# Optimization experiments

Measured on AMD Instinct MI355X. Metric: run time of the kernel, lower is better.

The kernel has to match this reference:

```python
import jax, jax.numpy as jnp
import numpy as np

N = 50000      # nodes
E = 800000     # edges (before self loops)
IN = 128       # in_channels
HID = 64       # hidden_channels
HEADS = 4      # num_heads
OUT = 40       # out_channels
NEG_SLOPE = 0.2


def setup_inputs() -> dict:
    key = jax.random.key(0)
    ks = jax.random.split(key, 16)
    x = jax.random.normal(ks[0], (N, IN), dtype=jnp.float32)
    edge_index = jax.random.randint(ks[1], (2, E), 0, N, dtype=jnp.int64)

    def lin(k, fan_in, fan_out):
        return jax.random.normal(k, (fan_in, fan_out), dtype=jnp.float32) * (1.0 / np.sqrt(fan_in))

    def att(k, h, c):
        return jax.random.normal(k, (h, c), dtype=jnp.float32) * (1.0 / np.sqrt(c))

    return {
        "x": x, "edge_index": edge_index,
        "W1": lin(ks[2], IN, HEADS * HID),
        "as1": att(ks[3], HEADS, HID), "ad1": att(ks[4], HEADS, HID),
        "b1": jnp.zeros((HEADS * HID,), jnp.float32),
        "W2": lin(ks[5], HEADS * HID, HEADS * HID),
        "as2": att(ks[6], HEADS, HID), "ad2": att(ks[7], HEADS, HID),
        "b2": jnp.zeros((HEADS * HID,), jnp.float32),
        "W3": lin(ks[8], HEADS * HID, OUT),
        "as3": att(ks[9], 1, OUT), "ad3": att(ks[10], 1, OUT),
        "b3": jnp.zeros((OUT,), jnp.float32),
    }


def _gat_layer(x, src, dst, W, a_src, a_dst, b):
    """One GATConv: linear -> per-edge attention -> segment softmax -> scatter-sum."""
    n = x.shape[0]
    H, C = a_src.shape
    h = (x @ W).reshape(n, H, C)                       # [N,H,C]
    al_s = jnp.einsum('nhc,hc->nh', h, a_src)          # [N,H]
    al_d = jnp.einsum('nhc,hc->nh', h, a_dst)          # [N,H]
    alpha = jax.nn.leaky_relu(al_s[src] + al_d[dst], NEG_SLOPE)  # [Etot,H]
    m = jax.ops.segment_max(alpha, dst, num_segments=n)          # stable softmax over incoming edges
    e = jnp.exp(alpha - m[dst])
    denom = jax.ops.segment_sum(e, dst, num_segments=n)
    attn = e / denom[dst]                              # [Etot,H]
    out = jax.ops.segment_sum(h[src] * attn[:, :, None], dst, num_segments=n)  # [N,H,C]
    return out.reshape(n, H * C) + b


def reference(x, edge_index, W1, as1, ad1, b1, W2, as2, ad2, b2, W3, as3, ad3, b3):
    # add self loops once (PyG GATConv default add_self_loops=True)
    loops = jnp.arange(N, dtype=edge_index.dtype)
    src = jnp.concatenate([edge_index[0], loops])
    dst = jnp.concatenate([edge_index[1], loops])

    h = _gat_layer(x, src, dst, W1, as1, ad1, b1)
    h = jax.nn.relu(h)                                 # dropout is identity in eval mode
    h = _gat_layer(h, src, dst, W2, as2, ad2, b2)
    h = jax.nn.relu(h)
    h = _gat_layer(h, src, dst, W3, as3, ad3, b3)      # final layer: 1 head
    return jax.nn.log_softmax(h, axis=-1)
```

## Files before the change

kernel.cpp:

```cpp
#include <hip/hip_runtime.h>
#include <math.h>

#define N_NODES 50000
#define N_EDGES 800000
#define ETOT    (N_EDGES + N_NODES)
#define EPAD_MAX 1200000
#define IN_CH   128
#define OUT_CH  40
#define NEG     0.2f
#define CAP     64

#define NPF   98
#define NFINE 512
#define FCAP  2400

typedef __attribute__((ext_vector_type(8))) short bf16x8;
typedef __attribute__((ext_vector_type(4))) float f32x4;
typedef __attribute__((ext_vector_type(2))) float f32x2;

__device__ inline unsigned short f2bf(float f) {
    unsigned int u = __float_as_uint(f);
    return (unsigned short)((u + 0x7FFFu + ((u >> 16) & 1u)) >> 16);
}
__device__ inline float bf2f(unsigned short u) {
    return __uint_as_float((unsigned int)u << 16);
}
__device__ inline float lrelu(float a) { return (a > 0.f) ? a : NEG * a; }

__global__ __launch_bounds__(256) void k_bkt(const int* __restrict__ ei,
                                             int* __restrict__ fcur,
                                             unsigned int* __restrict__ fbuf,
                                             const float* __restrict__ W1,
                                             const float* __restrict__ W2,
                                             const float* __restrict__ W3,
                                             unsigned short* __restrict__ Wt1,
                                             unsigned short* __restrict__ Wt2,
                                             unsigned short* __restrict__ Wt3) {
    if (blockIdx.x >= 256) {
        int i = (blockIdx.x - 256) * 256 + threadIdx.x;
        if (i < 32768) {
            int n = i >> 7, k = i & 127;
            Wt1[i] = f2bf(W1[(long)k * 256 + n]);
        } else if (i < 98304) {
            int j = i - 32768;
            int n = j >> 8, k = j & 255;
            Wt2[j] = f2bf(W2[(long)k * 256 + n]);
        } else if (i < 114688) {
            int j = i - 98304;
            int n = j >> 8, k = j & 255;
            Wt3[j] = (n < OUT_CH) ? f2bf(W3[(long)k * OUT_CH + n]) : (unsigned short)0;
        }
        return;
    }
    __shared__ int lcnt[NFINE], lbase[NFINE], lcur[NFINE];
    int tid = threadIdx.x;
    for (int i = tid; i < NFINE; i += 256) lcnt[i] = 0;
    __syncthreads();
    for (int i = blockIdx.x * 256 + tid; i < ETOT; i += 256 * 256) {
        int d = (i < N_EDGES) ? ei[N_EDGES + i] : (i - N_EDGES);
        atomicAdd(&lcnt[d / NPF], 1);
    }
    __syncthreads();
    for (int i = tid; i < NFINE; i += 256) {
        lbase[i] = atomicAdd(&fcur[i], lcnt[i]);
        lcur[i] = 0;
    }
    __syncthreads();
    for (int i = blockIdx.x * 256 + tid; i < ETOT; i += 256 * 256) {
        int s, d;
        if (i < N_EDGES) { s = ei[i]; d = ei[N_EDGES + i]; }
        else             { s = i - N_EDGES; d = s; }
        int p = d / NPF;
        int off = atomicAdd(&lcur[p], 1);
        fbuf[(long)p * FCAP + lbase[p] + off] = (unsigned int)s | ((unsigned int)d << 16);
    }
}

__global__ __launch_bounds__(256) void k_build(const int* __restrict__ fcur,
                                               const unsigned int* __restrict__ fbuf,
                                               int* __restrict__ deg,
                                               int* __restrict__ gcur,
                                               int* __restrict__ start,
                                               int* __restrict__ eSrc) {
    __shared__ int cnt[NPF];
    __shared__ int sval[128];
    __shared__ int offs[NPF];
    __shared__ int base_[NPF];
    __shared__ int pbase;
    int f = blockIdx.x;
    int tid = threadIdx.x;
    int n0 = f * NPF;
    int nend = min(n0 + NPF, N_NODES);
    int nn = nend - n0;
    if (tid < NPF) cnt[tid] = 0;
    __syncthreads();
    int n = fcur[f];
    for (int i = tid; i < n; i += 256)
        atomicAdd(&cnt[(int)(fbuf[(long)f * FCAP + i] >> 16) - n0], 1);
    __syncthreads();
    int pd = 0;
    if (tid < 128) {
        pd = (tid < nn) ? ((cnt[tid] + 7) & ~7) : 0;
        sval[tid] = pd;
    }
    __syncthreads();
    #pragma unroll
    for (int off = 1; off < 128; off <<= 1) {
        int t = 0;
        if (tid < 128 && tid >= off) t = sval[tid - off];
        __syncthreads();
        if (tid < 128) sval[tid] += t;
        __syncthreads();
    }
    if (tid == 0) pbase = atomicAdd(gcur, sval[127]);
    __syncthreads();
    if (tid < nn) {
        int st = pbase + sval[tid] - pd;
        deg[n0 + tid] = cnt[tid];
        start[n0 + tid] = st;
        offs[tid] = st;
        base_[tid] = st;
    }
    __syncthreads();
    for (int i = tid; i < n; i += 256) {
        unsigned int u = fbuf[(long)f * FCAP + i];
        int d = (int)(u >> 16);
        int pos = atomicAdd(&offs[d - n0], 1);
        eSrc[pos] = (int)(u & 0xFFFFu);
    }
    __syncthreads();
    if (tid < nn) {
        int endp = offs[tid];
        int dg = endp - base_[tid];
        int stop = base_[tid] + ((dg + 7) & ~7);
        for (int k2 = endp; k2 < stop; ++k2) eSrc[k2] = -1;
    }
}

#define PITCH 40
template<int BN, int FM, int FN, bool CVT, bool FP8OUT, bool L4>
__global__ __launch_bounds__(256) void k_mfma(const void* __restrict__ Araw,
                                              const unsigned short* __restrict__ Bt,
                                              void* __restrict__ Cout,
                                              const float* __restrict__ a_s,
                                              const float* __restrict__ a_d,
                                              float* __restrict__ als,
                                              float* __restrict__ ald,
                                              int M, int K, int Ncol) {
    __shared__ unsigned short As[128 * PITCH];
    __shared__ unsigned short Bs[BN * PITCH];
    const int WCOLS = BN / (FN * 16);
    int tid = threadIdx.x;
    int wave = tid >> 6, lane = tid & 63;
    int quad = lane >> 4, l16 = lane & 15;
    int wr = wave / WCOLS, wc = wave % WCOLS;
    long row0 = (long)blockIdx.x * 128;
    int col0 = blockIdx.y * BN;

    f32x4 acc[FM][FN] = {};

    for (int k0 = 0; k0 < K; k0 += 32) {
        for (int c = tid; c < 512; c += 256) {
            int r = c >> 2, kp = (c & 3) << 3;
            long gr = row0 + r;
            if (CVT) {
                const float* A32 = (const float*)Araw;
                ushort4 lo = {0,0,0,0}, hi = {0,0,0,0};
                if (gr < M) {
                    float4 v0 = *(const float4*)(A32 + gr * K + k0 + kp);
                    float4 v1 = *(const float4*)(A32 + gr * K + k0 + kp + 4);
                    lo.x = f2bf(v0.x); lo.y = f2bf(v0.y); lo.z = f2bf(v0.z); lo.w = f2bf(v0.w);
                    hi.x = f2bf(v1.x); hi.y = f2bf(v1.y); hi.z = f2bf(v1.z); hi.w = f2bf(v1.w);
                }
                *(ushort4*)(As + r * PITCH + kp) = lo;
                *(ushort4*)(As + r * PITCH + kp + 4) = hi;
            } else {
                const unsigned short* A16 = (const unsigned short*)Araw;
                uint4 v = {0u, 0u, 0u, 0u};
                if (gr < M) v = *(const uint4*)(A16 + gr * K + k0 + kp);
                *(uint4*)(As + r * PITCH + kp) = v;
            }
        }
        for (int c = tid; c < BN * 4; c += 256) {
            int r = c >> 2, kp = (c & 3) << 3;
            uint4 v = *(const uint4*)(Bt + (long)(col0 + r) * K + k0 + kp);
            *(uint4*)(Bs + r * PITCH + kp) = v;
        }
        __syncthreads();
        bf16x8 af[FM], bfr[FN];
        #pragma unroll
        for (int i = 0; i < FM; ++i)
            af[i] = *(const bf16x8*)(As + (wr * FM * 16 + i * 16 + l16) * PITCH + quad * 8);
        #pragma unroll
        for (int j = 0; j < FN; ++j)
            bfr[j] = *(const bf16x8*)(Bs + (wc * FN * 16 + j * 16 + l16) * PITCH + quad * 8);
        #pragma unroll
        for (int i = 0; i < FM; ++i)
            #pragma unroll
            for (int j = 0; j < FN; ++j)
                acc[i][j] = __builtin_amdgcn_mfma_f32_16x16x32_bf16(af[i], bfr[j], acc[i][j], 0, 0, 0);
        __syncthreads();
    }

    {
        int head = L4 ? (blockIdx.y * WCOLS + wc) : 0;
        float as_v[FN], ad_v[FN];
        #pragma unroll
        for (int j = 0; j < FN; ++j) {
            int cidx = j * 16 + l16;
            if (L4) {
                as_v[j] = a_s[head * 64 + cidx];
                ad_v[j] = a_d[head * 64 + cidx];
            } else {
                as_v[j] = (cidx < OUT_CH) ? a_s[cidx] : 0.f;
                ad_v[j] = (cidx < OUT_CH) ? a_d[cidx] : 0.f;
            }
        }
        #pragma unroll
        for (int i = 0; i < FM; ++i) {
            #pragma unroll
            for (int v = 0; v < 4; ++v) {
                float ps = acc[i][0][v] * as_v[0] + acc[i][1][v] * as_v[1]
                         + acc[i][2][v] * as_v[2] + acc[i][3][v] * as_v[3];
                float pd = acc[i][0][v] * ad_v[0] + acc[i][1][v] * ad_v[1]
                         + acc[i][2][v] * ad_v[2] + acc[i][3][v] * ad_v[3];
                #pragma unroll
                for (int off = 1; off < 16; off <<= 1) {
                    ps += __shfl_xor(ps, off);
                    pd += __shfl_xor(pd, off);
                }
                if (l16 == 0) {
                    long row = row0 + wr * (FM * 16) + i * 16 + quad * 4 + v;
                    if (row < M) {
                        if (L4) { als[row * 4 + head] = ps; ald[row * 4 + head] = pd; }
                        else    { als[row] = ps; ald[row] = pd; }
                    }
                }
            }
        }
    }

    if (FP8OUT) {
        unsigned char* C8 = (unsigned char*)Cout;
        #pragma unroll
        for (int i = 0; i < FM; ++i) {
            #pragma unroll
            for (int v = 0; v < 4; ++v) {
                long row = row0 + wr * FM * 16 + i * 16 + quad * 4 + v;
                if (row < M) {
                    int p01 = __builtin_amdgcn_cvt_pk_fp8_f32(acc[i][0][v], acc[i][1][v], 0, false);
                    int p23 = __builtin_amdgcn_cvt_pk_fp8_f32(acc[i][2][v], acc[i][3][v], 0, false);
                    unsigned char* b = C8 + row * 256 + col0 + wc * (FN * 16) + l16;
                    b[0]  = (unsigned char)(p01 & 0xFF);
                    b[16] = (unsigned char)((p01 >> 8) & 0xFF);
                    b[32] = (unsigned char)(p23 & 0xFF);
                    b[48] = (unsigned char)((p23 >> 8) & 0xFF);
                }
            }
        }
    } else {
        unsigned short* C = (unsigned short*)Cout;
        #pragma unroll
        for (int i = 0; i < FM; ++i) {
            long rowb = row0 + wr * FM * 16 + i * 16 + quad * 4;
            #pragma unroll
            for (int j = 0; j < FN; ++j) {
                int col = col0 + wc * FN * 16 + j * 16 + l16;
                if (col < Ncol) {
                    #pragma unroll
                    for (int v = 0; v < 4; ++v) {
                        long r = rowb + v;
                        if (r < M) C[r * Ncol + col] = f2bf(acc[i][j][v]);
                    }
                }
            }
        }
    }
}

__global__ __launch_bounds__(256) void k_agg4(const unsigned char* __restrict__ h8,
                                              const int* __restrict__ start,
                                              const int* __restrict__ deg,
                                              const int* __restrict__ eSrc,
                                              const float* __restrict__ als,
                                              const float* __restrict__ ald,
                                              const float* __restrict__ bias,
                                              unsigned short* __restrict__ out) {
    __shared__ float wbuf[4][CAP * 4];
    __shared__ int   sbuf[4][CAP];
    int wid = threadIdx.x >> 6;
    int node = (blockIdx.x * blockDim.x + threadIdx.x) >> 6;
    int lane = threadIdx.x & 63;
    if (node >= N_NODES) return;
    int st = start[node];
    int dgp = (deg[node] + 7) & ~7;
    const int* ep = eSrc + st;

    int l16 = lane & 15, headw = lane >> 4;
    float aldd4 = ald[node * 4 + headw];
    int ncap = (dgp < CAP) ? dgp : CAP;
    for (int c = 0; c < ncap; c += 16) {
        int slot = c + l16;
        bool ok = (slot < ncap);
        int raw = ok ? ep[slot] : -1;
        int ss = (raw < 0) ? 0 : raw;
        float a = als[(long)ss * 4 + headw] + aldd4;
        float w = (raw < 0) ? 0.f : __expf(lrelu(a));
        if (ok) {
            wbuf[wid][slot * 4 + headw] = w;
            if (headw == 0) sbuf[wid][slot] = ss << 8;
        }
    }

    int q = lane >> 4;
    int head = l16 >> 2;
    const unsigned char* hb = h8 + l16 * 16;
    float den = 0.f;
    f32x2 acc2[8] = {};

    for (int j = 0; j < ncap; j += 8) {
        int  s0 = sbuf[wid][j + q];
        int  s1 = sbuf[wid][j + 4 + q];
        float w0 = wbuf[wid][(j + q) * 4 + head];
        float w1 = wbuf[wid][(j + 4 + q) * 4 + head];
        uint4 h0 = *(const uint4*)(hb + (long)s0);
        uint4 h1 = *(const uint4*)(hb + (long)s1);
        den += w0 + w1;
        f32x2 W0; W0.x = w0; W0.y = w0;
        f32x2 W1; W1.x = w1; W1.y = w1;
        acc2[0] += W0 * __builtin_amdgcn_cvt_pk_f32_fp8((int)h0.x, false);
        acc2[1] += W0 * __builtin_amdgcn_cvt_pk_f32_fp8((int)h0.x, true);
        acc2[2] += W0 * __builtin_amdgcn_cvt_pk_f32_fp8((int)h0.y, false);
        acc2[3] += W0 * __builtin_amdgcn_cvt_pk_f32_fp8((int)h0.y, true);
        acc2[4] += W0 * __builtin_amdgcn_cvt_pk_f32_fp8((int)h0.z, false);
        acc2[5] += W0 * __builtin_amdgcn_cvt_pk_f32_fp8((int)h0.z, true);
        acc2[6] += W0 * __builtin_amdgcn_cvt_pk_f32_fp8((int)h0.w, false);
        acc2[7] += W0 * __builtin_amdgcn_cvt_pk_f32_fp8((int)h0.w, true);
        acc2[0] += W1 * __builtin_amdgcn_cvt_pk_f32_fp8((int)h1.x, false);
        acc2[1] += W1 * __builtin_amdgcn_cvt_pk_f32_fp8((int)h1.x, true);
        acc2[2] += W1 * __builtin_amdgcn_cvt_pk_f32_fp8((int)h1.y, false);
        acc2[3] += W1 * __builtin_amdgcn_cvt_pk_f32_fp8((int)h1.y, true);
        acc2[4] += W1 * __builtin_amdgcn_cvt_pk_f32_fp8((int)h1.z, false);
        acc2[5] += W1 * __builtin_amdgcn_cvt_pk_f32_fp8((int)h1.z, true);
        acc2[6] += W1 * __builtin_amdgcn_cvt_pk_f32_fp8((int)h1.w, false);
        acc2[7] += W1 * __builtin_amdgcn_cvt_pk_f32_fp8((int)h1.w, true);
    }

    if (dgp > ncap) {
        float alddq = ald[node * 4 + head];
        for (int j = ncap; j < dgp; j += 4) {
            int raw = ep[j + q];
            int ss = (raw < 0) ? 0 : raw;
            float w = (raw < 0) ? 0.f : __expf(lrelu(als[(long)ss * 4 + head] + alddq));
            uint4 hv = *(const uint4*)(h8 + ((long)ss << 8) + l16 * 16);
            den += w;
            f32x2 W0; W0.x = w; W0.y = w;
            acc2[0] += W0 * __builtin_amdgcn_cvt_pk_f32_fp8((int)hv.x, false);
            acc2[1] += W0 * __builtin_amdgcn_cvt_pk_f32_fp8((int)hv.x, true);
            acc2[2] += W0 * __builtin_amdgcn_cvt_pk_f32_fp8((int)hv.y, false);
            acc2[3] += W0 * __builtin_amdgcn_cvt_pk_f32_fp8((int)hv.y, true);
            acc2[4] += W0 * __builtin_amdgcn_cvt_pk_f32_fp8((int)hv.z, false);
            acc2[5] += W0 * __builtin_amdgcn_cvt_pk_f32_fp8((int)hv.z, true);
            acc2[6] += W0 * __builtin_amdgcn_cvt_pk_f32_fp8((int)hv.w, false);
            acc2[7] += W0 * __builtin_amdgcn_cvt_pk_f32_fp8((int)hv.w, true);
        }
    }

    den += __shfl_xor(den, 16);
    den += __shfl_xor(den, 32);
    #pragma unroll
    for (int c = 0; c < 8; ++c) {
        acc2[c].x += __shfl_xor(acc2[c].x, 16);
        acc2[c].y += __shfl_xor(acc2[c].y, 16);
        acc2[c].x += __shfl_xor(acc2[c].x, 32);
        acc2[c].y += __shfl_xor(acc2[c].y, 32);
    }

    if (q == 0) {
        float inv = 1.f / den;
        int cb = l16 * 16;
        float4 b0 = *(const float4*)(bias + cb);
        float4 b1 = *(const float4*)(bias + cb + 4);
        float4 b2 = *(const float4*)(bias + cb + 8);
        float4 b3 = *(const float4*)(bias + cb + 12);
        float v0  = fmaxf(acc2[0].x * inv + b0.x, 0.f);
        float v1  = fmaxf(acc2[0].y * inv + b0.y, 0.f);
        float v2  = fmaxf(acc2[1].x * inv + b0.z, 0.f);
        float v3  = fmaxf(acc2[1].y * inv + b0.w, 0.f);
        float v4  = fmaxf(acc2[2].x * inv + b1.x, 0.f);
        float v5  = fmaxf(acc2[2].y * inv + b1.y, 0.f);
        float v6  = fmaxf(acc2[3].x * inv + b1.z, 0.f);
        float v7  = fmaxf(acc2[3].y * inv + b1.w, 0.f);
        float v8  = fmaxf(acc2[4].x * inv + b2.x, 0.f);
        float v9  = fmaxf(acc2[4].y * inv + b2.y, 0.f);
        float v10 = fmaxf(acc2[5].x * inv + b2.z, 0.f);
        float v11 = fmaxf(acc2[5].y * inv + b2.w, 0.f);
        float v12 = fmaxf(acc2[6].x * inv + b3.x, 0.f);
        float v13 = fmaxf(acc2[6].y * inv + b3.y, 0.f);
        float v14 = fmaxf(acc2[7].x * inv + b3.z, 0.f);
        float v15 = fmaxf(acc2[7].y * inv + b3.w, 0.f);
        uint4 o0, o1;
        o0.x = (unsigned int)f2bf(v0)  | ((unsigned int)f2bf(v1)  << 16);
        o0.y = (unsigned int)f2bf(v2)  | ((unsigned int)f2bf(v3)  << 16);
        o0.z = (unsigned int)f2bf(v4)  | ((unsigned int)f2bf(v5)  << 16);
        o0.w = (unsigned int)f2bf(v6)  | ((unsigned int)f2bf(v7)  << 16);
        o1.x = (unsigned int)f2bf(v8)  | ((unsigned int)f2bf(v9)  << 16);
        o1.y = (unsigned int)f2bf(v10) | ((unsigned int)f2bf(v11) << 16);
        o1.z = (unsigned int)f2bf(v12) | ((unsigned int)f2bf(v13) << 16);
        o1.w = (unsigned int)f2bf(v14) | ((unsigned int)f2bf(v15) << 16);
        *(uint4*)(out + (long)node * 256 + cb) = o0;
        *(uint4*)(out + (long)node * 256 + cb + 8) = o1;
    }
}

__global__ __launch_bounds__(256) void k_agg1(const unsigned short* __restrict__ h,
                                              const int* __restrict__ start,
                                              const int* __restrict__ deg,
                                              const int* __restrict__ eSrc,
                                              const float* __restrict__ als,
                                              const float* __restrict__ ald,
                                              const float* __restrict__ bias,
                                              float* __restrict__ out) {
    int node = (blockIdx.x * blockDim.x + threadIdx.x) >> 6;
    int lane = threadIdx.x & 63;
    if (node >= N_NODES) return;
    int q = lane >> 4, r = lane & 15;
    bool act = (r < 10);
    int st = start[node];
    int dgp = (deg[node] + 7) & ~7;
    const int* ep = eSrc + st;
    float aldd = ald[node];

    float den = 0.f;
    float4 acc = {0.f, 0.f, 0.f, 0.f};

    int j = 0;
    for (; j + 16 <= dgp; j += 16) {
        int base = j + q * 4;
        int s[4];
        float w[4];
        #pragma unroll
        for (int u = 0; u < 4; ++u) s[u] = ep[base + u];
        #pragma unroll
        for (int u = 0; u < 4; ++u) {
            int raw = s[u];
            int ss = (raw < 0) ? 0 : raw;
            w[u] = (raw < 0) ? 0.f : __expf(lrelu(als[ss] + aldd));
            s[u] = ss;
        }
        ushort4 hh[4];
        #pragma unroll
        for (int u = 0; u < 4; ++u) {
            ushort4 t = {0, 0, 0, 0};
            if (act) t = *(const ushort4*)(h + (long)s[u] * OUT_CH + r * 4);
            hh[u] = t;
        }
        #pragma unroll
        for (int u = 0; u < 4; ++u) {
            den += w[u];
            acc.x += w[u] * bf2f(hh[u].x);
            acc.y += w[u] * bf2f(hh[u].y);
            acc.z += w[u] * bf2f(hh[u].z);
            acc.w += w[u] * bf2f(hh[u].w);
        }
    }
    if (j < dgp) {
        int base = j + q * 2;
        int s[2];
        float w[2];
        #pragma unroll
        for (int u = 0; u < 2; ++u) s[u] = ep[base + u];
        #pragma unroll
        for (int u = 0; u < 2; ++u) {
            int raw = s[u];
            int ss = (raw < 0) ? 0 : raw;
            w[u] = (raw < 0) ? 0.f : __expf(lrelu(als[ss] + aldd));
            s[u] = ss;
        }
        ushort4 hh[2];
        #pragma unroll
        for (int u = 0; u < 2; ++u) {
            ushort4 t = {0, 0, 0, 0};
            if (act) t = *(const ushort4*)(h + (long)s[u] * OUT_CH + r * 4);
            hh[u] = t;
        }
        #pragma unroll
        for (int u = 0; u < 2; ++u) {
            den += w[u];
            acc.x += w[u] * bf2f(hh[u].x);
            acc.y += w[u] * bf2f(hh[u].y);
            acc.z += w[u] * bf2f(hh[u].z);
            acc.w += w[u] * bf2f(hh[u].w);
        }
    }

    #pragma unroll
    for (int off = 16; off < 64; off <<= 1) {
        acc.x += __shfl_xor(acc.x, off);
        acc.y += __shfl_xor(acc.y, off);
        acc.z += __shfl_xor(acc.z, off);
        acc.w += __shfl_xor(acc.w, off);
        den   += __shfl_xor(den, off);
    }
    float inv = 1.f / den;
    float4 bv = {0.f, 0.f, 0.f, 0.f};
    if (act) bv = *(const float4*)(bias + r * 4);
    float4 v;
    v.x = acc.x * inv + bv.x;
    v.y = acc.y * inv + bv.y;
    v.z = acc.z * inv + bv.z;
    v.w = acc.w * inv + bv.w;
    float mx = act ? fmaxf(fmaxf(v.x, v.y), fmaxf(v.z, v.w)) : -INFINITY;
    #pragma unroll
    for (int off = 1; off < 16; off <<= 1) mx = fmaxf(mx, __shfl_xor(mx, off));
    float sum = act ? (__expf(v.x - mx) + __expf(v.y - mx) + __expf(v.z - mx) + __expf(v.w - mx)) : 0.f;
    #pragma unroll
    for (int off = 1; off < 16; off <<= 1) sum += __shfl_xor(sum, off);
    float lse = mx + logf(sum);
    if (q == 0 && act) {
        float4 o;
        o.x = v.x - lse;
        o.y = v.y - lse;
        o.z = v.z - lse;
        o.w = v.w - lse;
        *(float4*)(out + (long)node * OUT_CH + r * 4) = o;
    }
}

extern "C" void kernel_launch(void* const* d_in, const int* in_sizes, int n_in,
                              void* d_out, int out_size, void* d_ws, size_t ws_size,
                              hipStream_t stream) {
    (void)in_sizes; (void)n_in; (void)out_size; (void)ws_size;
    const float* x   = (const float*)d_in[0];
    const int*   ei  = (const int*)d_in[1];
    const float* W1  = (const float*)d_in[2];
    const float* as1 = (const float*)d_in[3];
    const float* ad1 = (const float*)d_in[4];
    const float* b1  = (const float*)d_in[5];
    const float* W2  = (const float*)d_in[6];
    const float* as2 = (const float*)d_in[7];
    const float* ad2 = (const float*)d_in[8];
    const float* b2  = (const float*)d_in[9];
    const float* W3  = (const float*)d_in[10];
    const float* as3 = (const float*)d_in[11];
    const float* ad3 = (const float*)d_in[12];
    const float* b3  = (const float*)d_in[13];
    float* out = (float*)d_out;

    char* p = (char*)d_ws;
    auto alloc = [&](size_t b) { char* r = p; p += (b + 255) & ~(size_t)255; return r; };
    int*   deg   = (int*)alloc((size_t)N_NODES * 4);
    int*   start = (int*)alloc((size_t)N_NODES * 4);
    int*   psum  = (int*)alloc((size_t)NFINE * 4);
    int*   fcur  = (int*)alloc((size_t)NFINE * 4);
    unsigned int* fbuf = (unsigned int*)alloc((size_t)NFINE * FCAP * 4);
    int*   eSrc  = (int*)alloc((size_t)EPAD_MAX * 4);
    float* als   = (float*)alloc((size_t)N_NODES * 4 * 4);
    float* ald   = (float*)alloc((size_t)N_NODES * 4 * 4);
    unsigned char*  hA8  = (unsigned char*)alloc((size_t)N_NODES * 256);
    unsigned short* hBbf = (unsigned short*)alloc((size_t)N_NODES * 256 * 2);
    unsigned short* h3bf = (unsigned short*)alloc((size_t)N_NODES * OUT_CH * 2);
    unsigned short* Wt1  = (unsigned short*)alloc((size_t)256 * IN_CH * 2);
    unsigned short* Wt2  = (unsigned short*)alloc((size_t)256 * 256 * 2);
    unsigned short* Wt3  = (unsigned short*)alloc((size_t)64 * 256 * 2);

    const int WB = (N_NODES + 3) / 4;
    const int MB = (N_NODES + 127) / 128;

    hipMemsetAsync(psum, 0, (size_t)NFINE * 8, stream);
    k_bkt<<<256 + 448, 256, 0, stream>>>(ei, fcur, fbuf, W1, W2, W3, Wt1, Wt2, Wt3);
    k_build<<<NFINE, 256, 0, stream>>>(fcur, fbuf, deg, psum, start, eSrc);

    k_mfma<128, 4, 4, true, true, true><<<dim3(MB, 2), 256, 0, stream>>>(
        x, Wt1, hA8, as1, ad1, als, ald, N_NODES, IN_CH, 256);
    k_agg4<<<WB, 256, 0, stream>>>(hA8, start, deg, eSrc, als, ald, b1, hBbf);

    k_mfma<128, 4, 4, false, true, true><<<dim3(MB, 2), 256, 0, stream>>>(
        hBbf, Wt2, hA8, as2, ad2, als, ald, N_NODES, 256, 256);
    k_agg4<<<WB, 256, 0, stream>>>(hA8, start, deg, eSrc, als, ald, b2, hBbf);

    k_mfma<64, 2, 4, false, false, false><<<dim3(MB, 1), 256, 0, stream>>>(
        hBbf, Wt3, h3bf, as3, ad3, als, ald, N_NODES, 256, OUT_CH);
    k_agg1<<<WB, 256, 0, stream>>>(h3bf, start, deg, eSrc, als, ald, b3, out);
}
```

Baseline: 314.2 us.

## Fuse layer-1 GEMM into edge-bucketing kernel to overlap independent work

Moves the first-layer MFMA GEMM into the same launch as edge bucketing and W2/W3 conversion, dispatching by block index so the independent stages run concurrently. W1 conversion is split into a small preceding kernel, since the GEMM needs it. This removes a serialization point between graph preprocessing and the first feature transform. The combined kernel allocates the union of shared memory for both roles, which may reduce occupancy for the bucketing blocks.

Result: no change. 311.4 us (-0.9%).

```diff
diff --git a/kernel.cpp b/kernel.cpp
--- a/kernel.cpp
+++ b/kernel.cpp
@@ -14,6 +14,8 @@
 #define NFINE 512
 #define FCAP  2400
 
+#define MBLK  ((N_NODES + 127) / 128)
+
 typedef __attribute__((ext_vector_type(8))) short bf16x8;
 typedef __attribute__((ext_vector_type(4))) float f32x4;
 typedef __attribute__((ext_vector_type(2))) float f32x2;
@@ -27,126 +29,24 @@
 }
 __device__ inline float lrelu(float a) { return (a > 0.f) ? a : NEG * a; }
 
-__global__ __launch_bounds__(256) void k_bkt(const int* __restrict__ ei,
-                                             int* __restrict__ fcur,
-                                             unsigned int* __restrict__ fbuf,
-                                             const float* __restrict__ W1,
-                                             const float* __restrict__ W2,
-                                             const float* __restrict__ W3,
-                                             unsigned short* __restrict__ Wt1,
-                                             unsigned short* __restrict__ Wt2,
-                                             unsigned short* __restrict__ Wt3) {
-    if (blockIdx.x >= 256) {
-        int i = (blockIdx.x - 256) * 256 + threadIdx.x;
-        if (i < 32768) {
-            int n = i >> 7, k = i & 127;
-            Wt1[i] = f2bf(W1[(long)k * 256 + n]);
-        } else if (i < 98304) {
-            int j = i - 32768;
-            int n = j >> 8, k = j & 255;
-            Wt2[j] = f2bf(W2[(long)k * 256 + n]);
-        } else if (i < 114688) {
-            int j = i - 98304;
-            int n = j >> 8, k = j & 255;
-            Wt3[j] = (n < OUT_CH) ? f2bf(W3[(long)k * OUT_CH + n]) : (unsigned short)0;
-        }
-        return;
-    }
-    __shared__ int lcnt[NFINE], lbase[NFINE], lcur[NFINE];
-    int tid = threadIdx.x;
-    for (int i = tid; i < NFINE; i += 256) lcnt[i] = 0;
-    __syncthreads();
-    for (int i = blockIdx.x * 256 + tid; i < ETOT; i += 256 * 256) {
-        int d = (i < N_EDGES) ? ei[N_EDGES + i] : (i - N_EDGES);
-        atomicAdd(&lcnt[d / NPF], 1);
-    }
-    __syncthreads();
-    for (int i = tid; i < NFINE; i += 256) {
-        lbase[i] = atomicAdd(&fcur[i], lcnt[i]);
-        lcur[i] = 0;
-    }
-    __syncthreads();
-    for (int i = blockIdx.x * 256 + tid; i < ETOT; i += 256 * 256) {
-        int s, d;
-        if (i < N_EDGES) { s = ei[i]; d = ei[N_EDGES + i]; }
-        else             { s = i - N_EDGES; d = s; }
-        int p = d / NPF;
-        int off = atomicAdd(&lcur[p], 1);
-        fbuf[(long)p * FCAP + lbase[p] + off] = (unsigned int)s | ((unsigned int)d << 16);
-    }
-}
-
-__global__ __launch_bounds__(256) void k_build(const int* __restrict__ fcur,
-                                               const unsigned int* __restrict__ fbuf,
-                                               int* __restrict__ deg,
-                                               int* __restrict__ gcur,
-                                               int* __restrict__ start,
-                                               int* __restrict__ eSrc) {
-    __shared__ int cnt[NPF];
-    __shared__ int sval[128];
-    __shared__ int offs[NPF];
-    __shared__ int base_[NPF];
-    __shared__ int pbase;
-    int f = blockIdx.x;
-    int tid = threadIdx.x;
-    int n0 = f * NPF;
-    int nend = min(n0 + NPF, N_NODES);
-    int nn = nend - n0;
-    if (tid < NPF) cnt[tid] = 0;
-    __syncthreads();
-    int n = fcur[f];
-    for (int i = tid; i < n; i += 256)
-        atomicAdd(&cnt[(int)(fbuf[(long)f * FCAP + i] >> 16) - n0], 1);
-    __syncthreads();
-    int pd = 0;
-    if (tid < 128) {
-        pd = (tid < nn) ? ((cnt[tid] + 7) & ~7) : 0;
-        sval[tid] = pd;
-    }
-    __syncthreads();
-    #pragma unroll
-    for (int off = 1; off < 128; off <<= 1) {
-        int t = 0;
-        if (tid < 128 && tid >= off) t = sval[tid - off];
-        __syncthreads();
-        if (tid < 128) sval[tid] += t;
-        __syncthreads();
-    }
-    if (tid == 0) pbase = atomicAdd(gcur, sval[127]);
-    __syncthreads();
-    if (tid < nn) {
-        int st = pbase + sval[tid] - pd;
-        deg[n0 + tid] = cnt[tid];
-        start[n0 + tid] = st;
-        offs[tid] = st;
-        base_[tid] = st;
-    }
-    __syncthreads();
-    for (int i = tid; i < n; i += 256) {
-        unsigned int u = fbuf[(long)f * FCAP + i];
-        int d = (int)(u >> 16);
-        int pos = atomicAdd(&offs[d - n0], 1);
-        eSrc[pos] = (int)(u & 0xFFFFu);
-    }
-    __syncthreads();
-    if (tid < nn) {
-        int endp = offs[tid];
-        int dg = endp - base_[tid];
-        int stop = base_[tid] + ((dg + 7) & ~7);
-        for (int k2 = endp; k2 < stop; ++k2) eSrc[k2] = -1;
-    }
+__global__ __launch_bounds__(256) void k_wt1(const float* __restrict__ W1,
+                                             unsigned short* __restrict__ Wt1) {
+    int i = blockIdx.x * 256 + threadIdx.x;
+    int n = i >> 7, k = i & 127;
+    Wt1[i] = f2bf(W1[(long)k * 256 + n]);
 }
 
 #define PITCH 40
 template<int BN, int FM, int FN, bool CVT, bool FP8OUT, bool L4>
-__global__ __launch_bounds__(256) void k_mfma(const void* __restrict__ Araw,
-                                              const unsigned short* __restrict__ Bt,
-                                              void* __restrict__ Cout,
-                                              const float* __restrict__ a_s,
-                                              const float* __restrict__ a_d,
-                                              float* __restrict__ als,
-                                              float* __restrict__ ald,
-                                              int M, int K, int Ncol) {
+__device__ __forceinline__ void mfma_body(int bx, int by,
+                                          const void* __restrict__ Araw,
+                                          const unsigned short* __restrict__ Bt,
+                                          void* __restrict__ Cout,
+                                          const float* __restrict__ a_s,
+                                          const float* __restrict__ a_d,
+                                          float* __restrict__ als,
+                                          float* __restrict__ ald,
+                                          int M, int K, int Ncol) {
     __shared__ unsigned short As[128 * PITCH];
     __shared__ unsigned short Bs[BN * PITCH];
     const int WCOLS = BN / (FN * 16);
@@ -154,8 +54,8 @@
     int wave = tid >> 6, lane = tid & 63;
     int quad = lane >> 4, l16 = lane & 15;
     int wr = wave / WCOLS, wc = wave % WCOLS;
-    long row0 = (long)blockIdx.x * 128;
-    int col0 = blockIdx.y * BN;
+    long row0 = (long)bx * 128;
+    int col0 = by * BN;
 
     f32x4 acc[FM][FN] = {};
 
@@ -203,7 +103,7 @@
     }
 
     {
-        int head = L4 ? (blockIdx.y * WCOLS + wc) : 0;
+        int head = L4 ? (by * WCOLS + wc) : 0;
         float as_v[FN], ad_v[FN];
         #pragma unroll
         for (int j = 0; j < FN; ++j) {
@@ -275,6 +175,138 @@
                 }
             }
         }
+    }
+}
+
+template<int BN, int FM, int FN, bool CVT, bool FP8OUT, bool L4>
+__global__ __launch_bounds__(256) void k_mfma(const void* __restrict__ Araw,
+                                              const unsigned short* __restrict__ Bt,
+                                              void* __restrict__ Cout,
+                                              const float* __restrict__ a_s,
+                                              const float* __restrict__ a_d,
+                                              float* __restrict__ als,
+                                              float* __restrict__ ald,
+                                              int M, int K, int Ncol) {
+    mfma_body<BN, FM, FN, CVT, FP8OUT, L4>(blockIdx.x, blockIdx.y,
+                                           Araw, Bt, Cout, a_s, a_d, als, ald, M, K, Ncol);
+}
+
+__global__ __launch_bounds__(256) void k_front(const int* __restrict__ ei,
+                                               int* __restrict__ fcur,
+                                               unsigned int* __restrict__ fbuf,
+                                               const float* __restrict__ W2,
+                                               const float* __restrict__ W3,
+                                               unsigned short* __restrict__ Wt2,
+                                               unsigned short* __restrict__ Wt3,
+                                               const float* __restrict__ x,
+                                               const unsigned short* __restrict__ Wt1,
+                                               unsigned char* __restrict__ hA8,
+                                               const float* __restrict__ as1,
+                                               const float* __restrict__ ad1,
+                                               float* __restrict__ als,
+                                               float* __restrict__ ald) {
+    int b = blockIdx.x;
+    if (b >= 576) {
+        int g = b - 576;
+        mfma_body<128, 4, 4, true, true, true>(g % MBLK, g / MBLK,
+                                               x, Wt1, hA8, as1, ad1, als, ald,
+                                               N_NODES, IN_CH, 256);
+        return;
+    }
+    if (b >= 256) {
+        int j = (b - 256) * 256 + threadIdx.x;
+        if (j < 65536) {
+            int n = j >> 8, k = j & 255;
+            Wt2[j] = f2bf(W2[(long)k * 256 + n]);
+        } else {
+            int jj = j - 65536;
+            int n = jj >> 8, k = jj & 255;
+            Wt3[jj] = (n < OUT_CH) ? f2bf(W3[(long)k * OUT_CH + n]) : (unsigned short)0;
+        }
+        return;
+    }
+    __shared__ int lcnt[NFINE], lbase[NFINE], lcur[NFINE];
+    int tid = threadIdx.x;
+    for (int i = tid; i < NFINE; i += 256) lcnt[i] = 0;
+    __syncthreads();
+    for (int i = b * 256 + tid; i < ETOT; i += 256 * 256) {
+        int d = (i < N_EDGES) ? ei[N_EDGES + i] : (i - N_EDGES);
+        atomicAdd(&lcnt[d / NPF], 1);
+    }
+    __syncthreads();
+    for (int i = tid; i < NFINE; i += 256) {
+        lbase[i] = atomicAdd(&fcur[i], lcnt[i]);
+        lcur[i] = 0;
+    }
+    __syncthreads();
+    for (int i = b * 256 + tid; i < ETOT; i += 256 * 256) {
+        int s, d;
+        if (i < N_EDGES) { s = ei[i]; d = ei[N_EDGES + i]; }
+        else             { s = i - N_EDGES; d = s; }
+        int p = d / NPF;
+        int off = atomicAdd(&lcur[p], 1);
+        fbuf[(long)p * FCAP + lbase[p] + off] = (unsigned int)s | ((unsigned int)d << 16);
+    }
+}
+
+__global__ __launch_bounds__(256) void k_build(const int* __restrict__ fcur,
+                                               const unsigned int* __restrict__ fbuf,
+                                               int* __restrict__ deg,
+                                               int* __restrict__ gcur,
+                                               int* __restrict__ start,
+                                               int* __restrict__ eSrc) {
+    __shared__ int cnt[NPF];
+    __shared__ int sval[128];
+    __shared__ int offs[NPF];
+    __shared__ int base_[NPF];
+    __shared__ int pbase;
+    int f = blockIdx.x;
+    int tid = threadIdx.x;
+    int n0 = f * NPF;
+    int nend = min(n0 + NPF, N_NODES);
+    int nn = nend - n0;
+    if (tid < NPF) cnt[tid] = 0;
+    __syncthreads();
+    int n = fcur[f];
+    for (int i = tid; i < n; i += 256)
+        atomicAdd(&cnt[(int)(fbuf[(long)f * FCAP + i] >> 16) - n0], 1);
+    __syncthreads();
+    int pd = 0;
+    if (tid < 128) {
+        pd = (tid < nn) ? ((cnt[tid] + 7) & ~7) : 0;
+        sval[tid] = pd;
+    }
+    __syncthreads();
+    #pragma unroll
+    for (int off = 1; off < 128; off <<= 1) {
+        int t = 0;
+        if (tid < 128 && tid >= off) t = sval[tid - off];
+        __syncthreads();
+        if (tid < 128) sval[tid] += t;
+        __syncthreads();
+    }
+    if (tid == 0) pbase = atomicAdd(gcur, sval[127]);
+    __syncthreads();
+    if (tid < nn) {
+        int st = pbase + sval[tid] - pd;
+        deg[n0 + tid] = cnt[tid];
+        start[n0 + tid] = st;
+        offs[tid] = st;
+        base_[tid] = st;
+    }
+    __syncthreads();
+    for (int i = tid; i < n; i += 256) {
+        unsigned int u = fbuf[(long)f * FCAP + i];
+        int d = (int)(u >> 16);
+        int pos = atomicAdd(&offs[d - n0], 1);
+        eSrc[pos] = (int)(u & 0xFFFFu);
+    }
+    __syncthreads();
+    if (tid < nn) {
+        int endp = offs[tid];
+        int dg = endp - base_[tid];
+        int stop = base_[tid] + ((dg + 7) & ~7);
+        for (int k2 = endp; k2 < stop; ++k2) eSrc[k2] = -1;
     }
 }
 
@@ -565,21 +597,20 @@
     unsigned short* Wt3  = (unsigned short*)alloc((size_t)64 * 256 * 2);
 
     const int WB = (N_NODES + 3) / 4;
-    const int MB = (N_NODES + 127) / 128;
 
     hipMemsetAsync(psum, 0, (size_t)NFINE * 8, stream);
-    k_bkt<<<256 + 448, 256, 0, stream>>>(ei, fcur, fbuf, W1, W2, W3, Wt1, Wt2, Wt3);
+    k_wt1<<<128, 256, 0, stream>>>(W1, Wt1);
+    k_front<<<576 + 2 * MBLK, 256, 0, stream>>>(ei, fcur, fbuf, W2, W3, Wt2, Wt3,
+                                                x, Wt1, hA8, as1, ad1, als, ald);
     k_build<<<NFINE, 256, 0, stream>>>(fcur, fbuf, deg, psum, start, eSrc);
 
-    k_mfma<128, 4, 4, true, true, true><<<dim3(MB, 2), 256, 0, stream>>>(
-        x, Wt1, hA8, as1, ad1, als, ald, N_NODES, IN_CH, 256);
     k_agg4<<<WB, 256, 0, stream>>>(hA8, start, deg, eSrc, als, ald, b1, hBbf);
 
-    k_mfma<128, 4, 4, false, true, true><<<dim3(MB, 2), 256, 0, stream>>>(
+    k_mfma<128, 4, 4, false, true, true><<<dim3(MBLK, 2), 256, 0, stream>>>(
         hBbf, Wt2, hA8, as2, ad2, als, ald, N_NODES, 256, 256);
     k_agg4<<<WB, 256, 0, stream>>>(hA8, start, deg, eSrc, als, ald, b2, hBbf);
 
-    k_mfma<64, 2, 4, false, false, false><<<dim3(MB, 1), 256, 0, stream>>>(
+    k_mfma<64, 2, 4, false, false, false><<<dim3(MBLK, 1), 256, 0, stream>>>(
         hBbf, Wt3, h3bf, as3, ad3, als, ald, N_NODES, 256, OUT_CH);
     k_agg1<<<WB, 256, 0, stream>>>(h3bf, start, deg, eSrc, als, ald, b3, out);
 }
```
